# Kernel optimization log

Measured on AMD Instinct MI355X. Metric: run time of the kernel, lower is better.

Reference implementation:

```python
import jax, jax.numpy as jnp
import numpy as np

BS = 128      # batch
L = 512       # encoder sequence length
ENC = 512     # enc_hs
DEC = 1024    # dec_hs
ATTN = 512    # attn_sz
EMB = 256     # emb_sz
VOCAB = 128   # alphabet_size
MAX_LEN = 128 # text_max_len
SOS = 0


def setup_inputs() -> dict:
    key = jax.random.key(0)
    ks = jax.random.split(key, 10)
    s = 0.02
    return {
        "enc_out": jax.random.normal(ks[0], (BS, ENC, L), jnp.float32),
        # attention.encoder_conv (Conv1d enc->attn, kernel 1 == matmul)
        "W_enc": jax.random.normal(ks[1], (ATTN, ENC), jnp.float32) * s,
        "b_enc": jnp.zeros((ATTN,), jnp.float32),
        # attention.decoder_linear
        "W_dec": jax.random.normal(ks[2], (ATTN, DEC), jnp.float32) * s,
        "b_dec": jnp.zeros((ATTN,), jnp.float32),
        # attention.energy_layer (Conv1d attn->1, kernel 1)
        "v_e": jax.random.normal(ks[3], (ATTN,), jnp.float32) * s,
        "b_e": jnp.zeros((), jnp.float32),
        # embedding table
        "emb_table": jax.random.normal(ks[4], (VOCAB, EMB), jnp.float32) * s,
        # LSTM (single layer), PyTorch gate order i,f,g,o
        "W_ih": jax.random.normal(ks[5], (4 * DEC, EMB + ENC), jnp.float32) * s,
        "W_hh": jax.random.normal(ks[6], (4 * DEC, DEC), jnp.float32) * s,
        "b_ih": jnp.zeros((4 * DEC,), jnp.float32),
        "b_hh": jnp.zeros((4 * DEC,), jnp.float32),
        # output projection
        "W_out": jax.random.normal(ks[7], (VOCAB, DEC), jnp.float32) * s,
        "b_out": jnp.zeros((VOCAB,), jnp.float32),
    }


def reference(enc_out, W_enc, b_enc, W_dec, b_dec, v_e, b_e, emb_table,
              W_ih, W_hh, b_ih, b_hh, W_out, b_out):
    bs = enc_out.shape[0]
    # encoder_conv applied once: [bs, attn, L]
    weighted_enc = jnp.einsum('ae,bel->bal', W_enc, enc_out) + b_enc[None, :, None]

    def step(carry, _):
        x_idx, h, c = carry
        emb_x = emb_table[x_idx]                                   # [bs, emb]
        # Bahdanau attention
        wdec = h @ W_dec.T + b_dec                                 # [bs, attn]
        pre = jnp.tanh(weighted_enc + wdec[:, :, None])            # [bs, attn, L]
        scores = jnp.einsum('bal,a->bl', pre, v_e) + b_e           # [bs, L]
        alphas = jax.nn.softmax(scores, axis=-1)                   # [bs, L]
        context = jnp.einsum('bel,bl->be', enc_out, alphas)        # [bs, enc]
        # LSTM cell (PyTorch gate order i, f, g, o)
        rnn_x = jnp.concatenate([emb_x, context], axis=1)          # [bs, emb+enc]
        gates = rnn_x @ W_ih.T + b_ih + h @ W_hh.T + b_hh          # [bs, 4*dec]
        i, f, g, o = jnp.split(gates, 4, axis=1)
        i = jax.nn.sigmoid(i); f = jax.nn.sigmoid(f)
        g = jnp.tanh(g); o = jax.nn.sigmoid(o)
        c_new = f * c + i * g
        h_new = o * jnp.tanh(c_new)
        logits = h_new @ W_out.T + b_out                           # [bs, vocab]
        logp = jax.nn.log_softmax(logits, axis=-1)
        next_word = jnp.argmax(logp, axis=1).astype(jnp.int32)
        return (next_word, h_new, c_new), (logp, next_word, alphas)

    x0 = jnp.full((bs,), SOS, dtype=jnp.int32)
    h0 = jnp.zeros((bs, DEC), enc_out.dtype)
    c0 = jnp.zeros((bs, DEC), enc_out.dtype)
    _, (logp, preds, attn) = jax.lax.scan(step, (x0, h0, c0), None, length=MAX_LEN)
    # [T,bs,*] -> [bs,T,*]
    return logp.transpose(1, 0, 2), preds.transpose(1, 0), attn.transpose(1, 0, 2)
```

## Files before the change

### kernel.cpp

```cpp
#include <hip/hip_runtime.h>
#include <math.h>

#define BS 128
#define L 512
#define ENC 512
#define DEC 1024
#define ATTN 512
#define EMB 256
#define VOCAB 128
#define TMAX 128
#define KCAT 1792
#define G4 4096

#define OFF_WET    0ull
#define OFF_WGR    33554432ull
#define OFF_BGR    40894464ull
#define OFF_WOUTT  40898560ull
#define OFF_WDT    41029632ull
#define OFF_C      41553920ull
#define OFF_SCP    41684992ull
#define OFF_XCAT   41816064ull
#define OFF_GPART  42045440ull
#define OFF_FLAG   44142592ull

__device__ __forceinline__ float tanh_fast(float x) {
    float ax = fabsf(x);
    float e = __expf(-2.f * ax);
    float d = 1.f + e;
    float r = __builtin_amdgcn_rcpf(d);
    r = r * (2.f - d * r);
    float t = 1.f - 2.f * e * r;
    return copysignf(t, x);
}

__device__ __forceinline__ void pairsync(int* flag, int target) {
    __syncthreads();
    if (threadIdx.x == 0) {
        __threadfence();
        __hip_atomic_fetch_add(flag, 1, __ATOMIC_ACQ_REL, __HIP_MEMORY_SCOPE_AGENT);
        while (__hip_atomic_load(flag, __ATOMIC_RELAXED, __HIP_MEMORY_SCOPE_AGENT) < target) {
            __builtin_amdgcn_s_sleep(4);
        }
        __threadfence();
    }
    __syncthreads();
}

__global__ void k_prep(const float* __restrict__ W_ih, const float* __restrict__ W_hh,
                       const float* __restrict__ b_ih, const float* __restrict__ b_hh,
                       const float* __restrict__ W_out, const float* __restrict__ W_dec,
                       float* __restrict__ Wgr, float* __restrict__ bgr,
                       float* __restrict__ WoutT, float* __restrict__ WdT) {
    long i = (long)blockIdx.x * 256 + threadIdx.x;
    if (i < (long)G4 * KCAT) {
        int mp = (int)(i / KCAT), k = (int)(i % KCAT);
        int d = mp >> 2, g = mp & 3;
        int r = g * DEC + d;
        Wgr[i] = (k < EMB + ENC) ? W_ih[(long)r * (EMB + ENC) + k]
                                 : W_hh[(long)r * DEC + (k - (EMB + ENC))];
        return;
    }
    long j = i - (long)G4 * KCAT;
    if (j < G4) {
        int d = (int)(j >> 2), g = (int)(j & 3);
        int r = g * DEC + d;
        bgr[j] = b_ih[r] + b_hh[r];
        return;
    }
    long m = j - G4;
    if (m < (long)DEC * VOCAB) {
        int k = (int)(m / VOCAB), v = (int)(m % VOCAB);
        WoutT[m] = W_out[(long)v * DEC + k];
        return;
    }
    long p = m - (long)DEC * VOCAB;
    if (p < (long)DEC * ATTN) {
        int k = (int)(p / ATTN), a = (int)(p % ATTN);
        WdT[p] = W_dec[(long)a * DEC + k];
    }
}

__global__ void k_init(const float* __restrict__ emb_table,
                       float* __restrict__ c, float* __restrict__ Xcat,
                       int* __restrict__ flags) {
    long i = (long)blockIdx.x * 256 + threadIdx.x;
    if (i < BS * 16) flags[i] = 0;
    if (i < BS * DEC) { c[i] = 0.f; return; }
    long j = i - BS * DEC;
    if (j < (long)BS * KCAT) {
        int cdx = (int)(j % KCAT);
        Xcat[j] = (cdx < EMB) ? emb_table[cdx] : 0.f;
    }
}

__global__ __launch_bounds__(256) void k_wenc(const float* __restrict__ W_enc,
                                              const float* __restrict__ b_enc,
                                              const float* __restrict__ enc_out,
                                              float* __restrict__ weT) {
    __shared__ float As[16][68];
    __shared__ float Bs[16][68];
    int b = blockIdx.z;
    int a0 = blockIdx.y * 64;
    int l0 = blockIdx.x * 64;
    int t = threadIdx.x;
    int ty = t >> 4, tx = t & 15;
    float acc[4][4] = {};
    for (int e0 = 0; e0 < ENC; e0 += 16) {
        {
            int ar = t >> 2;
            int kg = (t & 3) << 2;
            float4 w4 = *(const float4*)&W_enc[(size_t)(a0 + ar) * ENC + e0 + kg];
            As[kg + 0][ar] = w4.x; As[kg + 1][ar] = w4.y; As[kg + 2][ar] = w4.z; As[kg + 3][ar] = w4.w;
            int er = t >> 4;
            int lg = (t & 15) << 2;
            float4 x4 = *(const float4*)&enc_out[((size_t)b * ENC + e0 + er) * L + l0 + lg];
            *(float4*)&Bs[er][lg] = x4;
        }
        __syncthreads();
        #pragma unroll
        for (int kk = 0; kk < 16; kk++) {
            float4 a4 = *(const float4*)&As[kk][ty * 4];
            float4 x4 = *(const float4*)&Bs[kk][tx * 4];
            float av[4] = {a4.x, a4.y, a4.z, a4.w};
            float xv[4] = {x4.x, x4.y, x4.z, x4.w};
            #pragma unroll
            for (int i = 0; i < 4; i++)
                #pragma unroll
                for (int j = 0; j < 4; j++) acc[i][j] += av[i] * xv[j];
        }
        __syncthreads();
    }
    float be0 = b_enc[a0 + ty * 4 + 0];
    float be1 = b_enc[a0 + ty * 4 + 1];
    float be2 = b_enc[a0 + ty * 4 + 2];
    float be3 = b_enc[a0 + ty * 4 + 3];
    #pragma unroll
    for (int j = 0; j < 4; j++) {
        int l = l0 + tx * 4 + j;
        float4 o = {acc[0][j] + be0, acc[1][j] + be1, acc[2][j] + be2, acc[3][j] + be3};
        *(float4*)&weT[((size_t)b * L + l) * ATTN + a0 + ty * 4] = o;
    }
}

__global__ __launch_bounds__(512) void k_aof(const float* __restrict__ gpart,
                                             const float* __restrict__ bgr,
                                             const float* __restrict__ WoutT,
                                             const float* __restrict__ b_out,
                                             const float* __restrict__ emb_table,
                                             const float* __restrict__ WdT,
                                             const float* __restrict__ b_dec,
                                             float* __restrict__ c,
                                             float* __restrict__ logp_out,
                                             float* __restrict__ preds_out,
                                             float* __restrict__ Xcat,
                                             const float* __restrict__ weT,
                                             const float* __restrict__ v_e,
                                             const float* __restrict__ b_e,
                                             const float* __restrict__ enc_out,
                                             float* __restrict__ attn_out,
                                             float* __restrict__ scp,
                                             int* __restrict__ flags, int ts) {
    __shared__ float hs[DEC];
    __shared__ float wd_l[256];
    __shared__ float vel[256];
    __shared__ float al[L];
    __shared__ float red[512];
    __shared__ float rv[128];
    __shared__ int ri[128];
    __shared__ float redw[256][2];
    int b = blockIdx.x >> 1, h = blockIdx.x & 1;
    int t = threadIdx.x;
    int* flag = flags + b * 16;
    int msync = (ts == 0) ? 0 : (2 * ts - 1);

    if (ts > 0) {
        float cold0 = c[(size_t)b * DEC + t];
        float cold1 = c[(size_t)b * DEC + 512 + t];
        pairsync(flag, 2 * (++msync));
        #pragma unroll
        for (int q = 0; q < 2; q++) {
            int d = q * 512 + t;
            const float* gp = gpart + (size_t)b * G4 + d * 4;
            float4 g = *(const float4*)gp;
            #pragma unroll
            for (int ks = 1; ks < 4; ks++) {
                float4 p = *(const float4*)(gp + (size_t)ks * BS * G4);
                g.x += p.x; g.y += p.y; g.z += p.z; g.w += p.w;
            }
            float4 bb = *(const float4*)&bgr[(size_t)d * 4];
            float gi = g.x + bb.x, gf = g.y + bb.y, gg = g.z + bb.z, go = g.w + bb.w;
            float fi = 1.f / (1.f + expf(-gi));
            float ff = 1.f / (1.f + expf(-gf));
            float fg = tanhf(gg);
            float fo = 1.f / (1.f + expf(-go));
            float cold = q ? cold1 : cold0;
            float cn = ff * cold + fi * fg;
            float hn = fo * tanhf(cn);
            if (h == 0) {
                c[(size_t)b * DEC + d] = cn;
                Xcat[(size_t)b * KCAT + EMB + ENC + d] = hn;
            }
            hs[d] = hn;
        }
        __syncthreads();
        if (h == 0) {
            int v = t & 127, kh = t >> 7;
            const float* wp = WoutT + (size_t)kh * 256 * VOCAB + v;
            float acc = 0.f;
            #pragma unroll 8
            for (int k = 0; k < 256; k++) acc += wp[(size_t)k * VOCAB] * hs[kh * 256 + k];
            red[t] = acc;
            __syncthreads();
            float logits = 0.f;
            if (t < 128) {
                logits = ((red[t] + red[t + 128]) + (red[t + 256] + red[t + 384])) + b_out[t];
                rv[t] = logits; ri[t] = t;
            }
            __syncthreads();
            for (int s = 64; s; s >>= 1) {
                if (t < s) {
                    float ov = rv[t + s]; int oi = ri[t + s];
                    if (ov > rv[t] || (ov == rv[t] && oi < ri[t])) { rv[t] = ov; ri[t] = oi; }
                }
                __syncthreads();
            }
            float m = rv[0]; int am = ri[0];
            __syncthreads();
            if (t < 128) red[t] = expf(logits - m);
            __syncthreads();
            for (int s = 64; s; s >>= 1) { if (t < s && t + s < 128) red[t] += red[t + s]; __syncthreads(); }
            if (t < 128) logp_out[((size_t)b * TMAX + (ts - 1)) * VOCAB + t] = logits - m - logf(red[0]);
            if (t == 0) preds_out[(size_t)b * TMAX + (ts - 1)] = (float)am;
            if (t < 256) Xcat[(size_t)b * KCAT + t] = emb_table[(size_t)am * EMB + t];
        }
        if (ts == TMAX) return;
        {
            int a_l = t >> 1, ksub = t & 1;
            int a = h * 256 + a_l;
            const float* wdp = WdT + (size_t)(ksub * 512) * ATTN + a;
            float s = 0.f;
            #pragma unroll 16
            for (int k = 0; k < 512; k++) s += wdp[(size_t)k * ATTN] * hs[ksub * 512 + k];
            redw[a_l][ksub] = s;
        }
        __syncthreads();
        if (t < 256) {
            wd_l[t] = (redw[t][0] + redw[t][1]) + b_dec[h * 256 + t];
            vel[t] = v_e[h * 256 + t];
        }
    } else {
        if (t < 256) {
            wd_l[t] = b_dec[h * 256 + t];
            vel[t] = v_e[h * 256 + t];
        }
    }
    __syncthreads();

    {
        int ah = t & 1;
        #pragma unroll
        for (int rr = 0; rr < 2; rr++) {
            int l = rr * 256 + (t >> 1);
            const float* row = weT + ((size_t)b * L + l) * ATTN + h * 256 + ah * 128;
            float acc = 0.f;
            #pragma unroll 8
            for (int a4 = 0; a4 < 128; a4 += 4) {
                float4 x = *(const float4*)&row[a4];
                int a = ah * 128 + a4;
                acc += vel[a + 0] * tanh_fast(x.x + wd_l[a + 0]);
                acc += vel[a + 1] * tanh_fast(x.y + wd_l[a + 1]);
                acc += vel[a + 2] * tanh_fast(x.z + wd_l[a + 2]);
                acc += vel[a + 3] * tanh_fast(x.w + wd_l[a + 3]);
            }
            acc += __shfl_xor(acc, 1, 64);
            if (ah == 0) scp[((size_t)h * BS + b) * L + l] = acc;
        }
    }
    pairsync(flag, 2 * (++msync));

    float sc = scp[(size_t)b * L + t] + scp[((size_t)BS + b) * L + t] + b_e[0];
    red[t] = sc;
    __syncthreads();
    for (int s = 256; s; s >>= 1) { if (t < s) red[t] = fmaxf(red[t], red[t + s]); __syncthreads(); }
    float m = red[0];
    __syncthreads();
    float e = expf(sc - m);
    red[t] = e;
    __syncthreads();
    for (int s = 256; s; s >>= 1) { if (t < s) red[t] += red[t + s]; __syncthreads(); }
    float inv = 1.f / red[0];
    al[t] = e * inv;
    __syncthreads();
    if (h == 0) attn_out[((size_t)b * TMAX + ts) * L + t] = al[t];

    {
        int r2 = t >> 1, lh2 = (t & 1) * 256;
        int e_ = h * 256 + r2;
        const float* erow = enc_out + ((size_t)b * ENC + e_) * L + lh2;
        float cacc = 0.f;
        #pragma unroll 8
        for (int l4 = 0; l4 < 256; l4 += 4) {
            float4 x = *(const float4*)&erow[l4];
            float4 a4 = *(const float4*)&al[lh2 + l4];
            cacc += x.x * a4.x + x.y * a4.y + x.z * a4.z + x.w * a4.w;
        }
        cacc += __shfl_xor(cacc, 1, 64);
        if ((t & 1) == 0) Xcat[(size_t)b * KCAT + EMB + e_] = cacc;
    }
}

__global__ __launch_bounds__(256) void k_gates(const float* __restrict__ Wgr,
                                               const float* __restrict__ Xcat,
                                               float* __restrict__ gates_part) {
    __shared__ float As[16][68];
    __shared__ float Xs[16][36];
    int M0 = blockIdx.x * 64;
    int b0 = blockIdx.y * 32;
    int ks = blockIdx.z;
    int kbase = ks * 448, kend = kbase + 448;
    int t = threadIdx.x, ty = t >> 4, tx = t & 15;
    int r = t >> 2, kg = (t & 3) << 2;
    float acc[4][2] = {};
    float4 wreg = *(const float4*)&Wgr[(size_t)(M0 + r) * KCAT + kbase + kg];
    float4 xreg;
    if (t < 128) xreg = *(const float4*)&Xcat[(size_t)(b0 + r) * KCAT + kbase + kg];
    for (int k0 = kbase; k0 < kend; k0 += 16) {
        As[kg + 0][r] = wreg.x; As[kg + 1][r] = wreg.y; As[kg + 2][r] = wreg.z; As[kg + 3][r] = wreg.w;
        if (t < 128) {
            Xs[kg + 0][r] = xreg.x; Xs[kg + 1][r] = xreg.y; Xs[kg + 2][r] = xreg.z; Xs[kg + 3][r] = xreg.w;
        }
        __syncthreads();
        if (k0 + 16 < kend) {
            wreg = *(const float4*)&Wgr[(size_t)(M0 + r) * KCAT + k0 + 16 + kg];
            if (t < 128) xreg = *(const float4*)&Xcat[(size_t)(b0 + r) * KCAT + k0 + 16 + kg];
        }
        #pragma unroll
        for (int kk = 0; kk < 16; kk++) {
            float4 a4 = *(const float4*)&As[kk][ty * 4];
            float xb0 = Xs[kk][tx * 2], xb1 = Xs[kk][tx * 2 + 1];
            acc[0][0] += a4.x * xb0; acc[0][1] += a4.x * xb1;
            acc[1][0] += a4.y * xb0; acc[1][1] += a4.y * xb1;
            acc[2][0] += a4.z * xb0; acc[2][1] += a4.z * xb1;
            acc[3][0] += a4.w * xb0; acc[3][1] += a4.w * xb1;
        }
        __syncthreads();
    }
    float* gp = gates_part + (size_t)ks * BS * G4;
    #pragma unroll
    for (int j = 0; j < 2; j++) {
        float4 o = {acc[0][j], acc[1][j], acc[2][j], acc[3][j]};
        *(float4*)&gp[(size_t)(b0 + tx * 2 + j) * G4 + M0 + ty * 4] = o;
    }
}

extern "C" void kernel_launch(void* const* d_in, const int* in_sizes, int n_in,
                              void* d_out, int out_size, void* d_ws, size_t ws_size,
                              hipStream_t stream) {
    const float* enc_out = (const float*)d_in[0];
    const float* W_enc   = (const float*)d_in[1];
    const float* b_enc   = (const float*)d_in[2];
    const float* W_dec   = (const float*)d_in[3];
    const float* b_dec   = (const float*)d_in[4];
    const float* v_e     = (const float*)d_in[5];
    const float* b_e     = (const float*)d_in[6];
    const float* emb     = (const float*)d_in[7];
    const float* W_ih    = (const float*)d_in[8];
    const float* W_hh    = (const float*)d_in[9];
    const float* b_ih    = (const float*)d_in[10];
    const float* b_hh    = (const float*)d_in[11];
    const float* W_out   = (const float*)d_in[12];
    const float* b_out   = (const float*)d_in[13];

    float* ws    = (float*)d_ws;
    float* weT   = ws + OFF_WET;
    float* Wgr   = ws + OFF_WGR;
    float* bgr   = ws + OFF_BGR;
    float* WoutT = ws + OFF_WOUTT;
    float* WdT   = ws + OFF_WDT;
    float* c     = ws + OFF_C;
    float* scp   = ws + OFF_SCP;
    float* Xcat  = ws + OFF_XCAT;
    float* gpart = ws + OFF_GPART;
    int*   flags = (int*)(ws + OFF_FLAG);

    float* logp_out  = (float*)d_out;
    float* preds_out = logp_out + (size_t)BS * TMAX * VOCAB;
    float* attn_out  = preds_out + (size_t)BS * TMAX;

    {
        long n = (long)G4 * KCAT + G4 + (long)DEC * VOCAB + (long)DEC * ATTN;
        k_prep<<<(int)((n + 255) / 256), 256, 0, stream>>>(W_ih, W_hh, b_ih, b_hh, W_out, W_dec,
                                                           Wgr, bgr, WoutT, WdT);
    }
    {
        long n = (long)BS * DEC + (long)BS * KCAT;
        k_init<<<(int)((n + 255) / 256), 256, 0, stream>>>(emb, c, Xcat, flags);
    }
    k_wenc<<<dim3(8, 8, 128), 256, 0, stream>>>(W_enc, b_enc, enc_out, weT);

    for (int t = 0; t < TMAX; t++) {
        k_aof<<<256, 512, 0, stream>>>(gpart, bgr, WoutT, b_out, emb, WdT, b_dec, c,
                                       logp_out, preds_out, Xcat, weT, v_e, b_e,
                                       enc_out, attn_out, scp, flags, t);
        k_gates<<<dim3(64, 4, 4), 256, 0, stream>>>(Wgr, Xcat, gpart);
    }
    k_aof<<<256, 512, 0, stream>>>(gpart, bgr, WoutT, b_out, emb, WdT, b_dec, c,
                                   logp_out, preds_out, Xcat, weT, v_e, b_e,
                                   enc_out, attn_out, scp, flags, TMAX);
}
```

Measured before the change: 20.66 ms.

## Fuse LSTM cell into gates GEMM epilogue and defer logits past attention

The LSTM pointwise cell update moves out of the attention kernel and into the gates GEMM. The last split-K block for each tile, detected with an atomic counter, reduces the partial sums and writes c and h into a double-buffered Xcat. The attention kernel now only loads h, and the output projection, log-softmax and argmax are moved after the attention/context work, which removes one pair sync per step. This adds atomic counters and a ping-pong Xcat buffer. The epilogue is serialized on the last-arriving block, and ordering now depends on threadfence correctness.

```diff
diff --git a/kernel.cpp b/kernel.cpp
--- a/kernel.cpp
+++ b/kernel.cpp
@@ -19,9 +19,11 @@
 #define OFF_WDT    41029632ull
 #define OFF_C      41553920ull
 #define OFF_SCP    41684992ull
-#define OFF_XCAT   41816064ull
-#define OFF_GPART  42045440ull
-#define OFF_FLAG   44142592ull
+#define OFF_XCAT0  41816064ull
+#define OFF_XCAT1  42045440ull
+#define OFF_GPART  42274816ull
+#define OFF_FLAG   44371968ull
+#define OFF_GCNT   44374016ull
 
 __device__ __forceinline__ float tanh_fast(float x) {
     float ax = fabsf(x);
@@ -81,15 +83,16 @@
 }
 
 __global__ void k_init(const float* __restrict__ emb_table,
-                       float* __restrict__ c, float* __restrict__ Xcat,
-                       int* __restrict__ flags) {
+                       float* __restrict__ c, float* __restrict__ Xcat0,
+                       int* __restrict__ flags, int* __restrict__ gcnt) {
     long i = (long)blockIdx.x * 256 + threadIdx.x;
     if (i < BS * 16) flags[i] = 0;
+    if (i < 256 * 16) gcnt[i] = 0;
     if (i < BS * DEC) { c[i] = 0.f; return; }
     long j = i - BS * DEC;
     if (j < (long)BS * KCAT) {
         int cdx = (int)(j % KCAT);
-        Xcat[j] = (cdx < EMB) ? emb_table[cdx] : 0.f;
+        Xcat0[j] = (cdx < EMB) ? emb_table[cdx] : 0.f;
     }
 }
 
@@ -142,14 +145,11 @@
     }
 }
 
-__global__ __launch_bounds__(512) void k_aof(const float* __restrict__ gpart,
-                                             const float* __restrict__ bgr,
-                                             const float* __restrict__ WoutT,
+__global__ __launch_bounds__(512) void k_aof(const float* __restrict__ WoutT,
                                              const float* __restrict__ b_out,
                                              const float* __restrict__ emb_table,
                                              const float* __restrict__ WdT,
                                              const float* __restrict__ b_dec,
-                                             float* __restrict__ c,
                                              float* __restrict__ logp_out,
                                              float* __restrict__ preds_out,
                                              float* __restrict__ Xcat,
@@ -171,69 +171,44 @@
     int b = blockIdx.x >> 1, h = blockIdx.x & 1;
     int t = threadIdx.x;
     int* flag = flags + b * 16;
-    int msync = (ts == 0) ? 0 : (2 * ts - 1);
 
     if (ts > 0) {
-        float cold0 = c[(size_t)b * DEC + t];
-        float cold1 = c[(size_t)b * DEC + 512 + t];
-        pairsync(flag, 2 * (++msync));
-        #pragma unroll
-        for (int q = 0; q < 2; q++) {
-            int d = q * 512 + t;
-            const float* gp = gpart + (size_t)b * G4 + d * 4;
-            float4 g = *(const float4*)gp;
-            #pragma unroll
-            for (int ks = 1; ks < 4; ks++) {
-                float4 p = *(const float4*)(gp + (size_t)ks * BS * G4);
-                g.x += p.x; g.y += p.y; g.z += p.z; g.w += p.w;
-            }
-            float4 bb = *(const float4*)&bgr[(size_t)d * 4];
-            float gi = g.x + bb.x, gf = g.y + bb.y, gg = g.z + bb.z, go = g.w + bb.w;
-            float fi = 1.f / (1.f + expf(-gi));
-            float ff = 1.f / (1.f + expf(-gf));
-            float fg = tanhf(gg);
-            float fo = 1.f / (1.f + expf(-go));
-            float cold = q ? cold1 : cold0;
-            float cn = ff * cold + fi * fg;
-            float hn = fo * tanhf(cn);
+        const float* hsrc = Xcat + (size_t)b * KCAT + EMB + ENC;
+        hs[t] = hsrc[t];
+        hs[t + 512] = hsrc[t + 512];
+        __syncthreads();
+        if (ts == TMAX) {
             if (h == 0) {
-                c[(size_t)b * DEC + d] = cn;
-                Xcat[(size_t)b * KCAT + EMB + ENC + d] = hn;
-            }
-            hs[d] = hn;
-        }
-        __syncthreads();
-        if (h == 0) {
-            int v = t & 127, kh = t >> 7;
-            const float* wp = WoutT + (size_t)kh * 256 * VOCAB + v;
-            float acc = 0.f;
-            #pragma unroll 8
-            for (int k = 0; k < 256; k++) acc += wp[(size_t)k * VOCAB] * hs[kh * 256 + k];
-            red[t] = acc;
-            __syncthreads();
-            float logits = 0.f;
-            if (t < 128) {
-                logits = ((red[t] + red[t + 128]) + (red[t + 256] + red[t + 384])) + b_out[t];
-                rv[t] = logits; ri[t] = t;
-            }
-            __syncthreads();
-            for (int s = 64; s; s >>= 1) {
-                if (t < s) {
-                    float ov = rv[t + s]; int oi = ri[t + s];
-                    if (ov > rv[t] || (ov == rv[t] && oi < ri[t])) { rv[t] = ov; ri[t] = oi; }
+                int v = t & 127, kh = t >> 7;
+                const float* wp = WoutT + (size_t)kh * 256 * VOCAB + v;
+                float acc = 0.f;
+                #pragma unroll 8
+                for (int k = 0; k < 256; k++) acc += wp[(size_t)k * VOCAB] * hs[kh * 256 + k];
+                red[t] = acc;
+                __syncthreads();
+                float logits = 0.f;
+                if (t < 128) {
+                    logits = ((red[t] + red[t + 128]) + (red[t + 256] + red[t + 384])) + b_out[t];
+                    rv[t] = logits; ri[t] = t;
                 }
                 __syncthreads();
+                for (int s = 64; s; s >>= 1) {
+                    if (t < s) {
+                        float ov = rv[t + s]; int oi = ri[t + s];
+                        if (ov > rv[t] || (ov == rv[t] && oi < ri[t])) { rv[t] = ov; ri[t] = oi; }
+                    }
+                    __syncthreads();
+                }
+                float m = rv[0]; int am = ri[0];
+                __syncthreads();
+                if (t < 128) red[t] = expf(logits - m);
+                __syncthreads();
+                for (int s = 64; s; s >>= 1) { if (t < s && t + s < 128) red[t] += red[t + s]; __syncthreads(); }
+                if (t < 128) logp_out[((size_t)b * TMAX + (ts - 1)) * VOCAB + t] = logits - m - logf(red[0]);
+                if (t == 0) preds_out[(size_t)b * TMAX + (ts - 1)] = (float)am;
             }
-            float m = rv[0]; int am = ri[0];
-            __syncthreads();
-            if (t < 128) red[t] = expf(logits - m);
-            __syncthreads();
-            for (int s = 64; s; s >>= 1) { if (t < s && t + s < 128) red[t] += red[t + s]; __syncthreads(); }
-            if (t < 128) logp_out[((size_t)b * TMAX + (ts - 1)) * VOCAB + t] = logits - m - logf(red[0]);
-            if (t == 0) preds_out[(size_t)b * TMAX + (ts - 1)] = (float)am;
-            if (t < 256) Xcat[(size_t)b * KCAT + t] = emb_table[(size_t)am * EMB + t];
-        }
-        if (ts == TMAX) return;
+            return;
+        }
         {
             int a_l = t >> 1, ksub = t & 1;
             int a = h * 256 + a_l;
@@ -276,7 +251,7 @@
             if (ah == 0) scp[((size_t)h * BS + b) * L + l] = acc;
         }
     }
-    pairsync(flag, 2 * (++msync));
+    pairsync(flag, 2 * (ts + 1));
 
     float sc = scp[(size_t)b * L + t] + scp[((size_t)BS + b) * L + t] + b_e[0];
     red[t] = sc;
@@ -307,13 +282,50 @@
         cacc += __shfl_xor(cacc, 1, 64);
         if ((t & 1) == 0) Xcat[(size_t)b * KCAT + EMB + e_] = cacc;
     }
+
+    if (h == 0 && ts > 0) {
+        int v = t & 127, kh = t >> 7;
+        const float* wp = WoutT + (size_t)kh * 256 * VOCAB + v;
+        float acc = 0.f;
+        #pragma unroll 8
+        for (int k = 0; k < 256; k++) acc += wp[(size_t)k * VOCAB] * hs[kh * 256 + k];
+        __syncthreads();
+        red[t] = acc;
+        __syncthreads();
+        float logits = 0.f;
+        if (t < 128) {
+            logits = ((red[t] + red[t + 128]) + (red[t + 256] + red[t + 384])) + b_out[t];
+            rv[t] = logits; ri[t] = t;
+        }
+        __syncthreads();
+        for (int s = 64; s; s >>= 1) {
+            if (t < s) {
+                float ov = rv[t + s]; int oi = ri[t + s];
+                if (ov > rv[t] || (ov == rv[t] && oi < ri[t])) { rv[t] = ov; ri[t] = oi; }
+            }
+            __syncthreads();
+        }
+        float m2 = rv[0]; int am = ri[0];
+        __syncthreads();
+        if (t < 128) red[t] = expf(logits - m2);
+        __syncthreads();
+        for (int s = 64; s; s >>= 1) { if (t < s && t + s < 128) red[t] += red[t + s]; __syncthreads(); }
+        if (t < 128) logp_out[((size_t)b * TMAX + (ts - 1)) * VOCAB + t] = logits - m2 - logf(red[0]);
+        if (t == 0) preds_out[(size_t)b * TMAX + (ts - 1)] = (float)am;
+        if (t < 256) Xcat[(size_t)b * KCAT + t] = emb_table[(size_t)am * EMB + t];
+    }
 }
 
 __global__ __launch_bounds__(256) void k_gates(const float* __restrict__ Wgr,
                                                const float* __restrict__ Xcat,
-                                               float* __restrict__ gates_part) {
+                                               float* __restrict__ gates_part,
+                                               const float* __restrict__ bgr,
+                                               float* __restrict__ c,
+                                               float* __restrict__ XoutH,
+                                               int* __restrict__ gcnt, int step) {
     __shared__ float As[16][68];
     __shared__ float Xs[16][36];
+    __shared__ int isfin;
     int M0 = blockIdx.x * 64;
     int b0 = blockIdx.y * 32;
     int ks = blockIdx.z;
@@ -350,6 +362,42 @@
     for (int j = 0; j < 2; j++) {
         float4 o = {acc[0][j], acc[1][j], acc[2][j], acc[3][j]};
         *(float4*)&gp[(size_t)(b0 + tx * 2 + j) * G4 + M0 + ty * 4] = o;
+    }
+    __syncthreads();
+    if (t == 0) {
+        __threadfence();
+        int tid = blockIdx.x * 4 + blockIdx.y;
+        int old = __hip_atomic_fetch_add(&gcnt[tid * 16], 1,
+                                         __ATOMIC_ACQ_REL, __HIP_MEMORY_SCOPE_AGENT);
+        isfin = (old == 4 * step + 3);
+        __threadfence();
+    }
+    __syncthreads();
+    if (!isfin) return;
+    int d0 = M0 >> 2;
+    #pragma unroll
+    for (int i = 0; i < 2; i++) {
+        int p = t + 256 * i;
+        int d = d0 + (p & 15);
+        int b = b0 + (p >> 4);
+        const float* gpp = gates_part + (size_t)b * G4 + d * 4;
+        float4 g = *(const float4*)gpp;
+        #pragma unroll
+        for (int k2 = 1; k2 < 4; k2++) {
+            float4 p4 = *(const float4*)(gpp + (size_t)k2 * BS * G4);
+            g.x += p4.x; g.y += p4.y; g.z += p4.z; g.w += p4.w;
+        }
+        float4 bb = *(const float4*)&bgr[(size_t)d * 4];
+        float gi = g.x + bb.x, gf = g.y + bb.y, gg = g.z + bb.z, go = g.w + bb.w;
+        float fi = 1.f / (1.f + expf(-gi));
+        float ff = 1.f / (1.f + expf(-gf));
+        float fg = tanhf(gg);
+        float fo = 1.f / (1.f + expf(-go));
+        size_t ix = (size_t)b * DEC + d;
+        float cn = ff * c[ix] + fi * fg;
+        float hn = fo * tanhf(cn);
+        c[ix] = cn;
+        XoutH[(size_t)b * KCAT + EMB + ENC + d] = hn;
     }
 }
 
@@ -379,9 +427,11 @@
     float* WdT   = ws + OFF_WDT;
     float* c     = ws + OFF_C;
     float* scp   = ws + OFF_SCP;
-    float* Xcat  = ws + OFF_XCAT;
+    float* xc0   = ws + OFF_XCAT0;
+    float* xc1   = ws + OFF_XCAT1;
     float* gpart = ws + OFF_GPART;
     int*   flags = (int*)(ws + OFF_FLAG);
+    int*   gcnt  = (int*)(ws + OFF_GCNT);
 
     float* logp_out  = (float*)d_out;
     float* preds_out = logp_out + (size_t)BS * TMAX * VOCAB;
@@ -394,17 +444,19 @@
     }
     {
         long n = (long)BS * DEC + (long)BS * KCAT;
-        k_init<<<(int)((n + 255) / 256), 256, 0, stream>>>(emb, c, Xcat, flags);
+        k_init<<<(int)((n + 255) / 256), 256, 0, stream>>>(emb, c, xc0, flags, gcnt);
     }
     k_wenc<<<dim3(8, 8, 128), 256, 0, stream>>>(W_enc, b_enc, enc_out, weT);
 
     for (int t = 0; t < TMAX; t++) {
-        k_aof<<<256, 512, 0, stream>>>(gpart, bgr, WoutT, b_out, emb, WdT, b_dec, c,
-                                       logp_out, preds_out, Xcat, weT, v_e, b_e,
+        float* xin  = (t & 1) ? xc1 : xc0;
+        float* xout = (t & 1) ? xc0 : xc1;
+        k_aof<<<256, 512, 0, stream>>>(WoutT, b_out, emb, WdT, b_dec,
+                                       logp_out, preds_out, xin, weT, v_e, b_e,
                                        enc_out, attn_out, scp, flags, t);
-        k_gates<<<dim3(64, 4, 4), 256, 0, stream>>>(Wgr, Xcat, gpart);
-    }
-    k_aof<<<256, 512, 0, stream>>>(gpart, bgr, WoutT, b_out, emb, WdT, b_dec, c,
-                                   logp_out, preds_out, Xcat, weT, v_e, b_e,
+        k_gates<<<dim3(64, 4, 4), 256, 0, stream>>>(Wgr, xin, gpart, bgr, c, xout, gcnt, t);
+    }
+    k_aof<<<256, 512, 0, stream>>>(WoutT, b_out, emb, WdT, b_dec,
+                                   logp_out, preds_out, xc0, weT, v_e, b_e,
                                    enc_out, attn_out, scp, flags, TMAX);
 }
```

Result: slower. 30.49 ms (+47.6%).
